# Kernel optimization log

Hardware: AMD Instinct MI355X
Metric: run time of the kernel (lower is better)

Reference implementation:

```python
import jax, jax.numpy as jnp
import numpy as np
import math

DIM = 128
B, S = 4, 4096


def setup_inputs() -> dict:
    key = jax.random.key(0)
    k1, k2, k3, k4 = jax.random.split(key, 4)
    inp = jax.random.normal(k1, (B, S, DIM), dtype=jnp.float32)
    w_k = jax.random.normal(k2, (DIM, DIM), dtype=jnp.float32) / math.sqrt(DIM)
    w_v = jax.random.normal(k3, (DIM, DIM), dtype=jnp.float32) / math.sqrt(DIM)
    mask = jax.random.randint(k4, (B, S, S), 0, 2).astype(jnp.bool_)
    return {"inp": inp, "w_k": w_k, "w_v": w_v, "mask": mask}


def reference(inp, w_k, w_v, mask):
    # key/val projections: BottleLinear(dim, dim, bias=False) -> x @ W^T
    key = jnp.einsum('bsd,ed->bse', inp, w_k)   # [B,S,D]
    val = jnp.einsum('bsd,ed->bse', inp, w_v)   # [B,S,D]
    # score = inp @ key^T / sqrt(dim)           # [B,S,S]
    score = jnp.einsum('bqd,bkd->bqk', inp, key) / math.sqrt(inp.shape[-1])
    score = jnp.where(mask, -jnp.inf, score)
    attn = jax.nn.softmax(score, axis=2)        # [B,S,S]
    out = jnp.einsum('bqk,bkd->bqd', attn, val) # [B,S,D]
    return (out, attn)
```

## Files before the change

### kernel.cpp

```cpp
#include <hip/hip_runtime.h>
#include <hip/hip_fp16.h>
#include <math.h>

#define DIM 128
#define SQL 4096
#define NBATCH 4
#define NROW (NBATCH*SQL)
#define SCALE 0.08838834764831845f
#define KSPLIT 8

typedef _Float16 f16;
typedef _Float16 f16x4 __attribute__((ext_vector_type(4)));
typedef _Float16 f16x8 __attribute__((ext_vector_type(8)));
typedef float f32x4 __attribute__((ext_vector_type(4)));

__device__ __forceinline__ f32x4 mfma16(f16x8 a, f16x8 b, f32x4 c) {
  return __builtin_amdgcn_mfma_f32_16x16x32_f16(a, b, c, 0, 0, 0);
}

__global__ __launch_bounds__(256) void maskpack(const void* __restrict__ mask,
                                                unsigned long long* __restrict__ mbits,
                                                int n) {
  __shared__ int s_is32;
  if (threadIdx.x == 0) {
    const unsigned int* w = (const unsigned int*)mask;
    int ok = 1;
    for (int i = 0; i < 64; ++i) ok &= (w[i] <= 1u);
    s_is32 = ok;
  }
  __syncthreads();
  const int t = threadIdx.x;
  const int stride = gridDim.x * blockDim.x;
  const uint4* mv = (const uint4*)mask;

  if (s_is32) {
    const int nvec = n >> 2;
    for (int i = blockIdx.x * blockDim.x + t; i < nvec; i += stride) {
      const uint4 v = mv[i];
      const unsigned int nib = (v.x != 0u) | ((v.y != 0u) << 1) |
                               ((v.z != 0u) << 2) | ((v.w != 0u) << 3);
      unsigned long long bits = (unsigned long long)nib << ((i & 15) * 4);
      bits |= __shfl_xor(bits, 1);
      bits |= __shfl_xor(bits, 2);
      bits |= __shfl_xor(bits, 4);
      bits |= __shfl_xor(bits, 8);
      if ((t & 15) == 0) mbits[i >> 4] = bits;
    }
  } else {
    const int nvec = n >> 4;
    for (int i = blockIdx.x * blockDim.x + t; i < nvec; i += stride) {
      const uint4 v = mv[i];
      const unsigned int M = 0x01020408u;
      unsigned int x;
      x = ((v.x | ((v.x & 0x7F7F7F7Fu) + 0x7F7F7F7Fu)) >> 7) & 0x01010101u;
      const unsigned int n0 = ((x * M) >> 24) & 0xFu;
      x = ((v.y | ((v.y & 0x7F7F7F7Fu) + 0x7F7F7F7Fu)) >> 7) & 0x01010101u;
      const unsigned int n1 = ((x * M) >> 24) & 0xFu;
      x = ((v.z | ((v.z & 0x7F7F7F7Fu) + 0x7F7F7F7Fu)) >> 7) & 0x01010101u;
      const unsigned int n2 = ((x * M) >> 24) & 0xFu;
      x = ((v.w | ((v.w & 0x7F7F7F7Fu) + 0x7F7F7F7Fu)) >> 7) & 0x01010101u;
      const unsigned int n3 = ((x * M) >> 24) & 0xFu;
      const unsigned int b16 = n0 | (n1 << 4) | (n2 << 8) | (n3 << 12);
      unsigned long long bits = (unsigned long long)b16 << ((i & 3) * 16);
      bits |= __shfl_xor(bits, 1);
      bits |= __shfl_xor(bits, 2);
      if ((t & 3) == 0) mbits[i >> 2] = bits;
    }
  }
}

__global__ __launch_bounds__(256) void proj(const float* __restrict__ inp,
                                            const float* __restrict__ wk,
                                            const float* __restrict__ wv,
                                            f16* __restrict__ q16,
                                            f16* __restrict__ kfrag,
                                            f16* __restrict__ vfrag) {
  __shared__ float s_in[16][DIM];
  __shared__ __align__(16) f16 s_vt[DIM][16];
  __shared__ __align__(16) f16 s_kf[2048];
  const int rowbase = blockIdx.x * 16;
  const int t = threadIdx.x;
  const int e = t & 127;
  const int half_ = t >> 7;

  for (int r = half_; r < 16; r += 2)
    s_in[r][e] = inp[(size_t)(rowbase + r) * DIM + e];
  __syncthreads();

  float ak[8], av[8];
#pragma unroll
  for (int i = 0; i < 8; ++i) { ak[i] = 0.f; av[i] = 0.f; }

  for (int d0 = 0; d0 < DIM; d0 += 8) {
    float wkl[8], wvl[8];
#pragma unroll
    for (int j = 0; j < 8; ++j) {
      wkl[j] = wk[(size_t)e * DIM + d0 + j];
      wvl[j] = wv[(size_t)e * DIM + d0 + j];
    }
#pragma unroll
    for (int i = 0; i < 8; ++i) {
      const int r = half_ * 8 + i;
#pragma unroll
      for (int j = 0; j < 8; ++j) {
        const float x = s_in[r][d0 + j];
        ak[i] += x * wkl[j];
        av[i] += x * wvl[j];
      }
    }
  }

  const int koff = (e >> 5) * 512 + ((e >> 3) & 3) * 128 + (e & 7);
#pragma unroll
  for (int i = 0; i < 8; ++i) {
    const int r = half_ * 8 + i;
    s_kf[koff + r * 8] = (f16)ak[i];
    q16[(size_t)(rowbase + r) * DIM + e] = (f16)s_in[r][e];
    s_vt[e][r] = (f16)av[i];
  }
  __syncthreads();

  *(f16x8*)(kfrag + ((size_t)(rowbase >> 4)) * 2048 + t * 8) =
      *(const f16x8*)&s_kf[t * 8];

  const int b    = rowbase / SQL;
  const int srow = rowbase % SQL;
  const int m    = (srow >> 4) & 3;
  const int kc2_ = m >> 1, qh = m & 1;
  const int dt_ = t >> 5, h8 = (t >> 4) & 1, l15_ = t & 15;
  const f16x8 vv = *(const f16x8*)&s_vt[dt_ * 16 + l15_][h8 * 8];
  *(f16x8*)(vfrag + ((size_t)b * 64 + (srow >> 6)) * 8192 +
            dt_ * 1024 + kc2_ * 512 + (2 * qh + h8) * 128 + l15_ * 8) = vv;
}

template<int SPILLF16>
__global__ __launch_bounds__(256) void fused(const f16* __restrict__ q16,
                                             const f16* __restrict__ kfrag,
                                             const f16* __restrict__ vfrag,
                                             const unsigned long long* __restrict__ mbits,
                                             float* __restrict__ lpart,
                                             float* __restrict__ opart,
                                             f16* __restrict__ p16,
                                             float* __restrict__ attn) {
  __shared__ __align__(16) f16 pbuf[4][16][72];
  const int kc      = blockIdx.x & (KSPLIT - 1);
  const int blkrow  = (blockIdx.x >> 3) * 64;
  const int b = blkrow / SQL;
  const int lane = threadIdx.x & 63;
  const int w = threadIdx.x >> 6;
  const int rowbase = blkrow + w * 16;
  const int l15 = lane & 15, quad = lane >> 4;

  f16x8 qa[4];
  {
    const f16* qp = q16 + (size_t)(rowbase + l15) * DIM + quad * 8;
#pragma unroll
    for (int c = 0; c < 4; ++c) qa[c] = *(const f16x8*)(qp + c * 32);
  }

  float l[4];
#pragma unroll
  for (int r = 0; r < 4; ++r) l[r] = 0.f;

  f32x4 oacc[8];
#pragma unroll
  for (int dt = 0; dt < 8; ++dt) oacc[dt] = (f32x4){0.f, 0.f, 0.f, 0.f};

  const f16* vf0 = vfrag + (size_t)b * 64 * 8192 + lane * 8;

  const int kb0 = kc * (SQL / KSPLIT);
  for (int kb = kb0; kb < kb0 + SQL / KSPLIT; kb += 64) {
    const size_t rt0 = (size_t)((b * SQL + kb) >> 4);
    f32x4 acc[4];
#pragma unroll
    for (int kt = 0; kt < 4; ++kt) {
      f32x4 a = {0.f, 0.f, 0.f, 0.f};
      const f16* kp = kfrag + (rt0 + kt) * 2048 + lane * 8;
#pragma unroll
      for (int c = 0; c < 4; ++c)
        a = mfma16(qa[c], *(const f16x8*)(kp + c * 512), a);
      acc[kt] = a;
    }
#pragma unroll
    for (int reg = 0; reg < 4; ++reg) {
      const int row = quad * 4 + reg;
      const int rg = rowbase + row;
      const unsigned long long mb = mbits[(size_t)rg * (SQL / 64) + (kb >> 6)];
#pragma unroll
      for (int kt = 0; kt < 4; ++kt) {
        float sv = acc[kt][reg] * SCALE;
        if ((mb >> (kt * 16 + l15)) & 1ull) sv = -1e30f;
        const float e = __expf(sv);
        l[reg] += e;
        pbuf[w][row][kt * 16 + l15] = (f16)e;
      }
    }
    if (SPILLF16) {
#pragma unroll
      for (int s = 0; s < 2; ++s) {
        const int r  = s * 8 + (lane >> 3);
        const int c0 = (lane & 7) * 8;
        const f16x8 v = *(const f16x8*)&pbuf[w][r][c0];
        __builtin_nontemporal_store(v, (f16x8*)(p16 + (size_t)(rowbase + r) * SQL + kb + c0));
      }
    } else {
#pragma unroll
      for (int s = 0; s < 4; ++s) {
        const int r  = s * 4 + (lane >> 4);
        const int c0 = (lane & 15) * 4;
        const f16x4 v = *(const f16x4*)&pbuf[w][r][c0];
        f32x4 o;
#pragma unroll
        for (int j = 0; j < 4; ++j) o[j] = (float)v[j];
        __builtin_nontemporal_store(o, (f32x4*)(attn + (size_t)(rowbase + r) * SQL + kb + c0));
      }
    }
    const f16* vft = vf0 + (size_t)(kb >> 6) * 8192;
#pragma unroll
    for (int kc2 = 0; kc2 < 2; ++kc2) {
      const f16x8 pa = *(const f16x8*)(&pbuf[w][l15][kc2 * 32 + quad * 8]);
#pragma unroll
      for (int dt = 0; dt < 8; ++dt)
        oacc[dt] = mfma16(pa, *(const f16x8*)(vft + dt * 1024 + kc2 * 512), oacc[dt]);
    }
  }

#pragma unroll
  for (int reg = 0; reg < 4; ++reg) {
#pragma unroll
    for (int off = 1; off < 16; off <<= 1) l[reg] += __shfl_xor(l[reg], off);
    if (l15 == 0) lpart[(size_t)kc * NROW + rowbase + quad * 4 + reg] = l[reg];
  }
#pragma unroll
  for (int dt = 0; dt < 8; ++dt)
#pragma unroll
    for (int reg = 0; reg < 4; ++reg)
      opart[(size_t)kc * NROW * DIM +
            (size_t)(rowbase + quad * 4 + reg) * DIM + dt * 16 + l15] = oacc[dt][reg];
}

__global__ __launch_bounds__(256) void rowprep(const float* __restrict__ lpart,
                                               const float* __restrict__ opart,
                                               float* __restrict__ ilrow,
                                               float* __restrict__ out) {
  const int r = blockIdx.x * 2 + (threadIdx.x >> 7);
  const int d = threadIdx.x & 127;
  float s = 0.f;
#pragma unroll
  for (int kc = 0; kc < KSPLIT; ++kc) s += lpart[(size_t)kc * NROW + r];
  const float il = 1.f / s;
  float o = 0.f;
#pragma unroll
  for (int kc = 0; kc < KSPLIT; ++kc)
    o += opart[((size_t)kc * NROW + r) * DIM + d];
  out[(size_t)r * DIM + d] = o * il;
  if (d == 0) ilrow[r] = il;
}

template<int SPILLF16>
__global__ __launch_bounds__(256) void attnscale(const f16* __restrict__ p16,
                                                 const float* __restrict__ ilrow,
                                                 float* __restrict__ attn) {
  const long long stride = (long long)gridDim.x * blockDim.x;
  if (SPILLF16) {
    const long long nchunk = (long long)NROW * SQL / 8;
    const f16x8* src = (const f16x8*)p16;
    f32x4* dst = (f32x4*)attn;
    for (long long c = (long long)blockIdx.x * blockDim.x + threadIdx.x;
         c < nchunk; c += stride) {
      const float il = ilrow[c >> 9];
      const f16x8 v = __builtin_nontemporal_load(src + c);
      f32x4 a, b2;
      a[0] = (float)v[0] * il; a[1] = (float)v[1] * il;
      a[2] = (float)v[2] * il; a[3] = (float)v[3] * il;
      b2[0] = (float)v[4] * il; b2[1] = (float)v[5] * il;
      b2[2] = (float)v[6] * il; b2[3] = (float)v[7] * il;
      __builtin_nontemporal_store(a, dst + 2 * c);
      __builtin_nontemporal_store(b2, dst + 2 * c + 1);
    }
  } else {
    const long long nchunk = (long long)NROW * SQL / 4;
    f32x4* dst = (f32x4*)attn;
    for (long long c = (long long)blockIdx.x * blockDim.x + threadIdx.x;
         c < nchunk; c += stride) {
      const float il = ilrow[c >> 10];
      f32x4 v = dst[c];
      v[0] *= il; v[1] *= il; v[2] *= il; v[3] *= il;
      __builtin_nontemporal_store(v, dst + c);
    }
  }
}

extern "C" void kernel_launch(void* const* d_in, const int* in_sizes, int n_in,
                              void* d_out, int out_size, void* d_ws, size_t ws_size,
                              hipStream_t stream) {
  const float* inp  = (const float*)d_in[0];
  const float* wk   = (const float*)d_in[1];
  const float* wv   = (const float*)d_in[2];
  const void*  mask = d_in[3];

  float* out  = (float*)d_out;
  float* attn = out + (size_t)NROW * DIM;

  char* ws = (char*)d_ws;
  f16* q16   = (f16*)ws;
  f16* kfrag = q16 + (size_t)NROW * DIM;
  f16* vfrag = kfrag + (size_t)NROW * DIM;
  unsigned long long* mbits =
      (unsigned long long*)(vfrag + (size_t)NROW * DIM);
  char* p = (char*)mbits + (size_t)NROW * (SQL / 8);
  float* lpart = (float*)p; p += (size_t)KSPLIT * NROW * sizeof(float);
  float* ilrow = (float*)p; p += (size_t)NROW * sizeof(float);
  float* opart = (float*)p; p += (size_t)KSPLIT * NROW * DIM * sizeof(float);
  f16*   p16   = (f16*)p;
  const size_t need = (size_t)(p - ws) + (size_t)NROW * SQL * sizeof(f16);
  const bool spill = ws_size >= need;

  maskpack<<<8192, 256, 0, stream>>>(mask, mbits, NBATCH * SQL * SQL);
  proj<<<NROW / 16, 256, 0, stream>>>(inp, wk, wv, q16, kfrag, vfrag);
  if (spill) {
    fused<1><<<(NROW / 64) * KSPLIT, 256, 0, stream>>>(q16, kfrag, vfrag, mbits,
                                                       lpart, opart, p16, attn);
    rowprep<<<NROW / 2, 256, 0, stream>>>(lpart, opart, ilrow, out);
    attnscale<1><<<2048, 256, 0, stream>>>(p16, ilrow, attn);
  } else {
    fused<0><<<(NROW / 64) * KSPLIT, 256, 0, stream>>>(q16, kfrag, vfrag, mbits,
                                                       lpart, opart, p16, attn);
    rowprep<<<NROW / 2, 256, 0, stream>>>(lpart, opart, ilrow, out);
    attnscale<0><<<2048, 256, 0, stream>>>(p16, ilrow, attn);
  }
}
```

Before: 650.4 us.

## Merge projection and mask-pack kernels, halve key split, vectorize rowprep

Fuses the projection and mask bit-packing kernels into one launch, with block ranges dispatching to each role. This removes a launch and lets the two memory-bound phases overlap. It also halves the key-split factor of the fused attention kernel, which shrinks the partial-output traffic but gives fewer, longer blocks. rowprep now uses float4 loads with 8 rows per block, and the attnscale grid is doubled. The combined prep kernel reserves the projection's shared memory for the mask blocks too, which may lower occupancy for those blocks.

```diff
diff --git a/kernel.cpp b/kernel.cpp
--- a/kernel.cpp
+++ b/kernel.cpp
@@ -7,7 +7,9 @@
 #define NBATCH 4
 #define NROW (NBATCH*SQL)
 #define SCALE 0.08838834764831845f
-#define KSPLIT 8
+#define KSPLIT 4
+#define PROJBLK (NROW/16)
+#define MASKBLK 8192
 
 typedef _Float16 f16;
 typedef _Float16 f16x4 __attribute__((ext_vector_type(4)));
@@ -18,24 +20,91 @@
   return __builtin_amdgcn_mfma_f32_16x16x32_f16(a, b, c, 0, 0, 0);
 }
 
-__global__ __launch_bounds__(256) void maskpack(const void* __restrict__ mask,
-                                                unsigned long long* __restrict__ mbits,
-                                                int n) {
+__global__ __launch_bounds__(256) void prep(const float* __restrict__ inp,
+                                            const float* __restrict__ wk,
+                                            const float* __restrict__ wv,
+                                            const void* __restrict__ mask,
+                                            f16* __restrict__ q16,
+                                            f16* __restrict__ kfrag,
+                                            f16* __restrict__ vfrag,
+                                            unsigned long long* __restrict__ mbits,
+                                            int n) {
+  __shared__ float s_in[16][DIM];
+  __shared__ __align__(16) f16 s_vt[DIM][16];
+  __shared__ __align__(16) f16 s_kf[2048];
   __shared__ int s_is32;
-  if (threadIdx.x == 0) {
+  const int t = threadIdx.x;
+
+  if (blockIdx.x < PROJBLK) {
+    const int rowbase = blockIdx.x * 16;
+    const int e = t & 127;
+    const int half_ = t >> 7;
+
+    for (int r = half_; r < 16; r += 2)
+      s_in[r][e] = inp[(size_t)(rowbase + r) * DIM + e];
+    __syncthreads();
+
+    float ak[8], av[8];
+#pragma unroll
+    for (int i = 0; i < 8; ++i) { ak[i] = 0.f; av[i] = 0.f; }
+
+    for (int d0 = 0; d0 < DIM; d0 += 8) {
+      float wkl[8], wvl[8];
+#pragma unroll
+      for (int j = 0; j < 8; ++j) {
+        wkl[j] = wk[(size_t)e * DIM + d0 + j];
+        wvl[j] = wv[(size_t)e * DIM + d0 + j];
+      }
+#pragma unroll
+      for (int i = 0; i < 8; ++i) {
+        const int r = half_ * 8 + i;
+#pragma unroll
+        for (int j = 0; j < 8; ++j) {
+          const float x = s_in[r][d0 + j];
+          ak[i] += x * wkl[j];
+          av[i] += x * wvl[j];
+        }
+      }
+    }
+
+    const int koff = (e >> 5) * 512 + ((e >> 3) & 3) * 128 + (e & 7);
+#pragma unroll
+    for (int i = 0; i < 8; ++i) {
+      const int r = half_ * 8 + i;
+      s_kf[koff + r * 8] = (f16)ak[i];
+      q16[(size_t)(rowbase + r) * DIM + e] = (f16)s_in[r][e];
+      s_vt[e][r] = (f16)av[i];
+    }
+    __syncthreads();
+
+    *(f16x8*)(kfrag + ((size_t)(rowbase >> 4)) * 2048 + t * 8) =
+        *(const f16x8*)&s_kf[t * 8];
+
+    const int b    = rowbase / SQL;
+    const int srow = rowbase % SQL;
+    const int m    = (srow >> 4) & 3;
+    const int kc2_ = m >> 1, qh = m & 1;
+    const int dt_ = t >> 5, h8 = (t >> 4) & 1, l15_ = t & 15;
+    const f16x8 vv = *(const f16x8*)&s_vt[dt_ * 16 + l15_][h8 * 8];
+    *(f16x8*)(vfrag + ((size_t)b * 64 + (srow >> 6)) * 8192 +
+              dt_ * 1024 + kc2_ * 512 + (2 * qh + h8) * 128 + l15_ * 8) = vv;
+    return;
+  }
+
+  if (t == 0) {
     const unsigned int* w = (const unsigned int*)mask;
     int ok = 1;
     for (int i = 0; i < 64; ++i) ok &= (w[i] <= 1u);
     s_is32 = ok;
   }
   __syncthreads();
-  const int t = threadIdx.x;
-  const int stride = gridDim.x * blockDim.x;
+  const int mb_bid = blockIdx.x - PROJBLK;
+  const int stride = MASKBLK * 256;
   const uint4* mv = (const uint4*)mask;
 
   if (s_is32) {
     const int nvec = n >> 2;
-    for (int i = blockIdx.x * blockDim.x + t; i < nvec; i += stride) {
+    for (int i = mb_bid * 256 + t; i < nvec; i += stride) {
       const uint4 v = mv[i];
       const unsigned int nib = (v.x != 0u) | ((v.y != 0u) << 1) |
                                ((v.z != 0u) << 2) | ((v.w != 0u) << 3);
@@ -48,7 +117,7 @@
     }
   } else {
     const int nvec = n >> 4;
-    for (int i = blockIdx.x * blockDim.x + t; i < nvec; i += stride) {
+    for (int i = mb_bid * 256 + t; i < nvec; i += stride) {
       const uint4 v = mv[i];
       const unsigned int M = 0x01020408u;
       unsigned int x;
@@ -69,70 +138,6 @@
   }
 }
 
-__global__ __launch_bounds__(256) void proj(const float* __restrict__ inp,
-                                            const float* __restrict__ wk,
-                                            const float* __restrict__ wv,
-                                            f16* __restrict__ q16,
-                                            f16* __restrict__ kfrag,
-                                            f16* __restrict__ vfrag) {
-  __shared__ float s_in[16][DIM];
-  __shared__ __align__(16) f16 s_vt[DIM][16];
-  __shared__ __align__(16) f16 s_kf[2048];
-  const int rowbase = blockIdx.x * 16;
-  const int t = threadIdx.x;
-  const int e = t & 127;
-  const int half_ = t >> 7;
-
-  for (int r = half_; r < 16; r += 2)
-    s_in[r][e] = inp[(size_t)(rowbase + r) * DIM + e];
-  __syncthreads();
-
-  float ak[8], av[8];
-#pragma unroll
-  for (int i = 0; i < 8; ++i) { ak[i] = 0.f; av[i] = 0.f; }
-
-  for (int d0 = 0; d0 < DIM; d0 += 8) {
-    float wkl[8], wvl[8];
-#pragma unroll
-    for (int j = 0; j < 8; ++j) {
-      wkl[j] = wk[(size_t)e * DIM + d0 + j];
-      wvl[j] = wv[(size_t)e * DIM + d0 + j];
-    }
-#pragma unroll
-    for (int i = 0; i < 8; ++i) {
-      const int r = half_ * 8 + i;
-#pragma unroll
-      for (int j = 0; j < 8; ++j) {
-        const float x = s_in[r][d0 + j];
-        ak[i] += x * wkl[j];
-        av[i] += x * wvl[j];
-      }
-    }
-  }
-
-  const int koff = (e >> 5) * 512 + ((e >> 3) & 3) * 128 + (e & 7);
-#pragma unroll
-  for (int i = 0; i < 8; ++i) {
-    const int r = half_ * 8 + i;
-    s_kf[koff + r * 8] = (f16)ak[i];
-    q16[(size_t)(rowbase + r) * DIM + e] = (f16)s_in[r][e];
-    s_vt[e][r] = (f16)av[i];
-  }
-  __syncthreads();
-
-  *(f16x8*)(kfrag + ((size_t)(rowbase >> 4)) * 2048 + t * 8) =
-      *(const f16x8*)&s_kf[t * 8];
-
-  const int b    = rowbase / SQL;
-  const int srow = rowbase % SQL;
-  const int m    = (srow >> 4) & 3;
-  const int kc2_ = m >> 1, qh = m & 1;
-  const int dt_ = t >> 5, h8 = (t >> 4) & 1, l15_ = t & 15;
-  const f16x8 vv = *(const f16x8*)&s_vt[dt_ * 16 + l15_][h8 * 8];
-  *(f16x8*)(vfrag + ((size_t)b * 64 + (srow >> 6)) * 8192 +
-            dt_ * 1024 + kc2_ * 512 + (2 * qh + h8) * 128 + l15_ * 8) = vv;
-}
-
 template<int SPILLF16>
 __global__ __launch_bounds__(256) void fused(const f16* __restrict__ q16,
                                              const f16* __restrict__ kfrag,
@@ -144,7 +149,7 @@
                                              float* __restrict__ attn) {
   __shared__ __align__(16) f16 pbuf[4][16][72];
   const int kc      = blockIdx.x & (KSPLIT - 1);
-  const int blkrow  = (blockIdx.x >> 3) * 64;
+  const int blkrow  = (blockIdx.x >> 2) * 64;
   const int b = blkrow / SQL;
   const int lane = threadIdx.x & 63;
   const int w = threadIdx.x >> 6;
@@ -243,18 +248,21 @@
                                                const float* __restrict__ opart,
                                                float* __restrict__ ilrow,
                                                float* __restrict__ out) {
-  const int r = blockIdx.x * 2 + (threadIdx.x >> 7);
-  const int d = threadIdx.x & 127;
+  const int r  = blockIdx.x * 8 + (threadIdx.x >> 5);
+  const int d4 = (threadIdx.x & 31) * 4;
   float s = 0.f;
 #pragma unroll
   for (int kc = 0; kc < KSPLIT; ++kc) s += lpart[(size_t)kc * NROW + r];
   const float il = 1.f / s;
-  float o = 0.f;
-#pragma unroll
-  for (int kc = 0; kc < KSPLIT; ++kc)
-    o += opart[((size_t)kc * NROW + r) * DIM + d];
-  out[(size_t)r * DIM + d] = o * il;
-  if (d == 0) ilrow[r] = il;
+  f32x4 o = {0.f, 0.f, 0.f, 0.f};
+#pragma unroll
+  for (int kc = 0; kc < KSPLIT; ++kc) {
+    const f32x4 v = *(const f32x4*)&opart[((size_t)kc * NROW + r) * DIM + d4];
+    o[0] += v[0]; o[1] += v[1]; o[2] += v[2]; o[3] += v[3];
+  }
+  o[0] *= il; o[1] *= il; o[2] *= il; o[3] *= il;
+  *(f32x4*)&out[(size_t)r * DIM + d4] = o;
+  if ((threadIdx.x & 31) == 0) ilrow[r] = il;
 }
 
 template<int SPILLF16>
@@ -316,17 +324,18 @@
   const size_t need = (size_t)(p - ws) + (size_t)NROW * SQL * sizeof(f16);
   const bool spill = ws_size >= need;
 
-  maskpack<<<8192, 256, 0, stream>>>(mask, mbits, NBATCH * SQL * SQL);
-  proj<<<NROW / 16, 256, 0, stream>>>(inp, wk, wv, q16, kfrag, vfrag);
+  prep<<<PROJBLK + MASKBLK, 256, 0, stream>>>(inp, wk, wv, mask,
+                                              q16, kfrag, vfrag, mbits,
+                                              NBATCH * SQL * SQL);
   if (spill) {
     fused<1><<<(NROW / 64) * KSPLIT, 256, 0, stream>>>(q16, kfrag, vfrag, mbits,
                                                        lpart, opart, p16, attn);
-    rowprep<<<NROW / 2, 256, 0, stream>>>(lpart, opart, ilrow, out);
-    attnscale<1><<<2048, 256, 0, stream>>>(p16, ilrow, attn);
+    rowprep<<<NROW / 8, 256, 0, stream>>>(lpart, opart, ilrow, out);
+    attnscale<1><<<4096, 256, 0, stream>>>(p16, ilrow, attn);
   } else {
     fused<0><<<(NROW / 64) * KSPLIT, 256, 0, stream>>>(q16, kfrag, vfrag, mbits,
                                                        lpart, opart, p16, attn);
-    rowprep<<<NROW / 2, 256, 0, stream>>>(lpart, opart, ilrow, out);
-    attnscale<0><<<2048, 256, 0, stream>>>(p16, ilrow, attn);
-  }
-}
+    rowprep<<<NROW / 8, 256, 0, stream>>>(lpart, opart, ilrow, out);
+    attnscale<0><<<4096, 256, 0, stream>>>(p16, ilrow, attn);
+  }
+}
```

New measurement: 718.9 us. +10.5%, slower.
